# Kernel optimization log

Hardware: AMD Instinct MI355X
Metric: run time of the kernel (lower is better)

The kernel has to match this reference:

```python
import jax, jax.numpy as jnp
import numpy as np

NUM_HEADS = 32
HEAD_DIM = 128
HIDDEN = NUM_HEADS * HEAD_DIM  # 4096
PAGE_SIZE = 16
NUM_PHYS_PAGES = 512
CACHE_POS = 4096
BATCH = 32
SEQ = 1


def setup_inputs() -> dict:
    key = jax.random.key(0)
    ks = jax.random.split(key, 6)
    scale = 0.02
    x = jax.random.normal(ks[0], (BATCH, SEQ, HIDDEN), dtype=jnp.float32)
    w_qkv = jax.random.normal(ks[1], (HIDDEN, 3 * HIDDEN), dtype=jnp.float32) * scale
    b_qkv = jnp.zeros((3 * HIDDEN,), dtype=jnp.float32)
    w_proj = jax.random.normal(ks[2], (HIDDEN, HIDDEN), dtype=jnp.float32) * scale
    b_proj = jnp.zeros((HIDDEN,), dtype=jnp.float32)
    k_pages = jax.random.normal(ks[3], (NUM_PHYS_PAGES, PAGE_SIZE, NUM_HEADS, HEAD_DIM), dtype=jnp.float32)
    v_pages = jax.random.normal(ks[4], (NUM_PHYS_PAGES, PAGE_SIZE, NUM_HEADS, HEAD_DIM), dtype=jnp.float32)
    # logical page -> physical page mapping (page table for one request)
    page_table = jax.random.randint(ks[5], (CACHE_POS // PAGE_SIZE,), 0, NUM_PHYS_PAGES, dtype=jnp.int64)
    return {
        "x": x, "w_qkv": w_qkv, "b_qkv": b_qkv, "w_proj": w_proj, "b_proj": b_proj,
        "k_pages": k_pages, "v_pages": v_pages, "page_table": page_table,
        "cache_pos": CACHE_POS,
    }


def reference(x, w_qkv, b_qkv, w_proj, b_proj, k_pages, v_pages, page_table, cache_pos):
    B, S, H = x.shape
    # fused QKV projection
    qkv = x @ w_qkv + b_qkv                      # [B,S,3H]
    q, k, v = jnp.split(qkv, 3, axis=-1)
    q = q.reshape(B, S, NUM_HEADS, HEAD_DIM).transpose(0, 2, 1, 3)  # [B,Hh,S,D]
    k = k.reshape(B, S, NUM_HEADS, HEAD_DIM).transpose(0, 2, 1, 3)
    v = v.reshape(B, S, NUM_HEADS, HEAD_DIM).transpose(0, 2, 1, 3)

    # Paged KV-cache gather: position -> (physical page, local offset)
    pos = jnp.arange(cache_pos)                  # cache_pos is a static Python int
    phys = page_table[pos // PAGE_SIZE]          # [T]
    off = pos % PAGE_SIZE                        # [T]
    cached_k = k_pages[phys, off]                # [T, Hh, D]
    cached_v = v_pages[phys, off]                # [T, Hh, D]
    # [1,Hh,T,D], shared across batch (as in the torch expand)
    cached_k = jnp.transpose(cached_k, (1, 0, 2))[None]
    cached_v = jnp.transpose(cached_v, (1, 0, 2))[None]
    cached_k = jnp.broadcast_to(cached_k, (B,) + cached_k.shape[1:])
    cached_v = jnp.broadcast_to(cached_v, (B,) + cached_v.shape[1:])

    k_full = jnp.concatenate([cached_k, k], axis=2)  # [B,Hh,T+S,D]
    v_full = jnp.concatenate([cached_v, v], axis=2)

    scores = jnp.einsum('bhsd,bhtd->bhst', q, k_full) / (HEAD_DIM ** 0.5)
    attn = jax.nn.softmax(scores, axis=-1)
    out = jnp.einsum('bhst,bhtd->bhsd', attn, v_full)  # [B,Hh,S,D]
    out = out.transpose(0, 2, 1, 3).reshape(B, S, H)
    return out @ w_proj + b_proj
```

## Files before the change

### kernel.cpp

```cpp
#include <hip/hip_runtime.h>

typedef __attribute__((ext_vector_type(4))) float f32x4;
typedef __attribute__((ext_vector_type(8))) short short8;
typedef unsigned short u16;
typedef unsigned int u32;

#define HEADS 32
#define D 128
#define TCACHE 4096
#define HID 4096
#define QKVN 12288
#define TSPLIT 16
#define KPS (TCACHE / TSPLIT)
#define QKV_KSPLIT 4
#define PROJ_KSPLIT 8
#define SCALE 0.08838834764831845f
#define ARENA_W 10880

static __device__ __forceinline__ float bf2f(u16 u) {
  u32 v = ((u32)u) << 16;
  return __builtin_bit_cast(float, v);
}
static __device__ __forceinline__ u16 f2bf(float f) {
  u32 u = __builtin_bit_cast(u32, f);
  u += 0x7FFFu + ((u >> 16) & 1u);
  return (u16)(u >> 16);
}

template <bool BF>
static __device__ __forceinline__ short8 load8(const void* p, long idx) {
  if constexpr (BF) {
    return *(const short8*)((const u16*)p + idx);
  } else {
    const float* f = (const float*)p + idx;
    f32x4 a = *(const f32x4*)f;
    f32x4 b = *(const f32x4*)(f + 4);
    short8 r;
    r[0] = (short)f2bf(a[0]); r[1] = (short)f2bf(a[1]);
    r[2] = (short)f2bf(a[2]); r[3] = (short)f2bf(a[3]);
    r[4] = (short)f2bf(b[0]); r[5] = (short)f2bf(b[1]);
    r[6] = (short)f2bf(b[2]); r[7] = (short)f2bf(b[3]);
    return r;
  }
}
template <bool BF>
static __device__ __forceinline__ short ld1(const void* p, long idx) {
  if constexpr (BF) return (short)((const u16*)p)[idx];
  else return (short)f2bf(((const float*)p)[idx]);
}

__global__ void prep(const u32* __restrict__ x, const u32* __restrict__ raw,
                     int* __restrict__ flag, int* __restrict__ ptn) {
  if (blockIdx.x == 0) {
    __shared__ int cnt;
    if (threadIdx.x == 0) cnt = 0;
    __syncthreads();
    u32 v = x[threadIdx.x * 256];
    u32 e = (v >> 7) & 0xFF;
    if (e >= 110 && e <= 140) atomicAdd(&cnt, 1);
    __syncthreads();
    if (threadIdx.x == 0) *flag = (cnt >= 192) ? 1 : 0;
  } else {
    __shared__ int is64;
    if (threadIdx.x == 0) is64 = 1;
    __syncthreads();
    if (threadIdx.x < 128) {
      u32 odd = raw[2 * threadIdx.x + 1];
      if (odd != 0) atomicAnd(&is64, 0);
    }
    __syncthreads();
    if (is64) ptn[threadIdx.x] = (int)raw[2 * threadIdx.x];
    else ptn[threadIdx.x] = (int)raw[threadIdx.x];
  }
}

template <bool ABF, bool BBF>
static __device__ __forceinline__ void gemm_body(const void* __restrict__ A,
                                                 const void* __restrict__ B,
                                                 float* __restrict__ C, int K, int N) {
  int wave = threadIdx.x >> 6, lane = threadIdx.x & 63;
  int l16 = lane & 15, lg = lane >> 4;
  int n0 = blockIdx.x * 64 + wave * 16;
  int kper = K / gridDim.y;
  int k0 = blockIdx.y * kper;
  f32x4 acc0 = {0.f, 0.f, 0.f, 0.f}, acc1 = {0.f, 0.f, 0.f, 0.f};
  long arow0 = (long)l16 * K, arow1 = (long)(l16 + 16) * K;
#pragma unroll 4
  for (int kk = k0; kk < k0 + kper; kk += 32) {
    long kbase = kk + lg * 8;
    short8 a0 = load8<ABF>(A, arow0 + kbase);
    short8 a1 = load8<ABF>(A, arow1 + kbase);
    short8 bfr;
#pragma unroll
    for (int i = 0; i < 8; i++) bfr[i] = ld1<BBF>(B, (kbase + i) * (long)N + n0 + l16);
    acc0 = __builtin_amdgcn_mfma_f32_16x16x32_bf16(a0, bfr, acc0, 0, 0, 0);
    acc1 = __builtin_amdgcn_mfma_f32_16x16x32_bf16(a1, bfr, acc1, 0, 0, 0);
  }
  float* Co = C + (long)blockIdx.y * 32 * N;
#pragma unroll
  for (int i = 0; i < 4; i++) {
    int b = lg * 4 + i;
    Co[(long)b * N + n0 + l16] = acc0[i];
    Co[(long)(b + 16) * N + n0 + l16] = acc1[i];
  }
}

#define GPITCH 36
static __device__ __forceinline__ void gemm32_body(const float* __restrict__ A,
                                                   const float* __restrict__ B,
                                                   float* __restrict__ C, int K, int N,
                                                   u16* __restrict__ BtL,
                                                   u16* __restrict__ AtL) {
  int t = threadIdx.x;
  int wave = t >> 6, lane = t & 63, l16 = lane & 15, lg = lane >> 4;
  int kper = K / gridDim.y;
  int k0 = blockIdx.y * kper;
  int steps = kper >> 5;
  long n0 = (long)blockIdx.x * 64;
  int bk = (t >> 4) * 2;
  int bc = (t & 15) * 4;
  int am = t >> 3;
  int ak = (t & 7) * 4;
  f32x4 acc0 = {0.f, 0.f, 0.f, 0.f}, acc1 = {0.f, 0.f, 0.f, 0.f};
  f32x4 rb0, rb1, ra;

  auto LOADG = [&](int kk) {
    const float* Bp = B + (long)(k0 + kk + bk) * N + n0 + bc;
    rb0 = *(const f32x4*)Bp;
    rb1 = *(const f32x4*)(Bp + N);
    ra = *(const f32x4*)(A + (long)am * K + k0 + kk + ak);
  };
  auto STORE = [&](int buf) {
    u16* Bt = BtL + buf * (64 * GPITCH);
#pragma unroll
    for (int c = 0; c < 4; c++) {
      u32 w = (u32)f2bf(rb0[c]) | ((u32)f2bf(rb1[c]) << 16);
      *(u32*)(Bt + (bc + c) * GPITCH + bk) = w;
    }
    u16* At = AtL + buf * (32 * GPITCH);
    u32 w0 = (u32)f2bf(ra[0]) | ((u32)f2bf(ra[1]) << 16);
    u32 w1 = (u32)f2bf(ra[2]) | ((u32)f2bf(ra[3]) << 16);
    *(u32*)(At + am * GPITCH + ak) = w0;
    *(u32*)(At + am * GPITCH + ak + 2) = w1;
  };

  LOADG(0);
  STORE(0);
  __syncthreads();
  for (int s = 0; s < steps; s++) {
    int cur = s & 1;
    bool more = (s + 1 < steps);
    if (more) LOADG((s + 1) * 32);
    union { short8 s8; u32 w[4]; } bf, af0, af1;
    {
      const u32* bp = (const u32*)(BtL + cur * (64 * GPITCH) + ((wave * 16 + l16) * GPITCH + lg * 8));
      bf.w[0] = bp[0]; bf.w[1] = bp[1]; bf.w[2] = bp[2]; bf.w[3] = bp[3];
      const u32* a0p = (const u32*)(AtL + cur * (32 * GPITCH) + (l16 * GPITCH + lg * 8));
      af0.w[0] = a0p[0]; af0.w[1] = a0p[1]; af0.w[2] = a0p[2]; af0.w[3] = a0p[3];
      const u32* a1p = (const u32*)(AtL + cur * (32 * GPITCH) + ((l16 + 16) * GPITCH + lg * 8));
      af1.w[0] = a1p[0]; af1.w[1] = a1p[1]; af1.w[2] = a1p[2]; af1.w[3] = a1p[3];
    }
    acc0 = __builtin_amdgcn_mfma_f32_16x16x32_bf16(af0.s8, bf.s8, acc0, 0, 0, 0);
    acc1 = __builtin_amdgcn_mfma_f32_16x16x32_bf16(af1.s8, bf.s8, acc1, 0, 0, 0);
    if (more) STORE(cur ^ 1);
    __syncthreads();
  }
  float* Co = C + (long)blockIdx.y * 32 * N;
  long cw = n0 + wave * 16 + l16;
#pragma unroll
  for (int i = 0; i < 4; i++) {
    int b = lg * 4 + i;
    Co[(long)b * N + cw] = acc0[i];
    Co[(long)(b + 16) * N + cw] = acc1[i];
  }
}

__global__ __launch_bounds__(256) void qkv_gemm(const void* A, const void* B, float* C,
                                                const int* flag) {
  __shared__ u16 BtL[2 * 64 * GPITCH];
  __shared__ u16 AtL[2 * 32 * GPITCH];
  if (*flag) gemm_body<true, true>(A, B, C, HID, QKVN);
  else gemm32_body((const float*)A, (const float*)B, C, HID, QKVN, BtL, AtL);
}
__global__ __launch_bounds__(256) void proj_gemm(const void* Abf, const void* Af32,
                                                 const void* B, float* C, const int* flag) {
  __shared__ u16 BtL[2 * 64 * GPITCH];
  __shared__ u16 AtL[2 * 32 * GPITCH];
  if (*flag) gemm_body<true, true>(Abf, B, C, HID, HID);
  else gemm32_body((const float*)Af32, (const float*)B, C, HID, HID, BtL, AtL);
}

__global__ void qkv_fin(const float* __restrict__ C, const void* __restrict__ bias,
                        u16* __restrict__ out, const int* __restrict__ flag) {
  int idx = blockIdx.x * 256 + threadIdx.x;
  if (idx >= 32 * QKVN) return;
  int n = idx % QKVN;
  float s = 0.f;
#pragma unroll
  for (int sp = 0; sp < QKV_KSPLIT; sp++) s += C[(long)sp * 32 * QKVN + idx];
  float bv;
  if (*flag) bv = bf2f(((const u16*)bias)[n]);
  else bv = ((const float*)bias)[n];
  out[idx] = f2bf(s + bv);
}

__global__ void proj_fin(const float* __restrict__ C, const void* __restrict__ bias,
                         void* __restrict__ out, const int* __restrict__ flag) {
  int idx = blockIdx.x * 256 + threadIdx.x;
  if (idx >= 32 * HID) return;
  int n = idx % HID;
  float s = 0.f;
#pragma unroll
  for (int sp = 0; sp < PROJ_KSPLIT; sp++) s += C[(long)sp * 32 * HID + idx];
  if (*flag) {
    s += bf2f(((const u16*)bias)[n]);
    ((u16*)out)[idx] = f2bf(s);
  } else {
    s += ((const float*)bias)[n];
    ((float*)out)[idx] = s;
  }
}

template <bool BF>
static __device__ __forceinline__ void attn_body(const u16* __restrict__ qkv,
                                                 const void* __restrict__ kp,
                                                 const void* __restrict__ vp,
                                                 const int* __restrict__ pt,
                                                 float* __restrict__ Op,
                                                 float* __restrict__ mp,
                                                 float* __restrict__ lp,
                                                 char* __restrict__ arena,
                                                 float (*mL)[32], float (*lL)[32]) {
  int split = blockIdx.x, h = blockIdx.y;
  int wave = threadIdx.x >> 6, lane = threadIdx.x & 63;
  int l16 = lane & 15, lg = lane >> 4;
  u16* VLw = (u16*)(arena + wave * ARENA_W);
  u16* pldsw = (u16*)(arena + wave * ARENA_W + 8320);

  short8 qf[2][4];
#pragma unroll
  for (int mt = 0; mt < 2; mt++)
#pragma unroll
    for (int ks = 0; ks < 4; ks++)
      qf[mt][ks] = *(const short8*)(qkv + (long)(l16 + 16 * mt) * QKVN + h * D + ks * 32 + lg * 8);

  f32x4 acc[2][8];
#pragma unroll
  for (int mt = 0; mt < 2; mt++)
#pragma unroll
    for (int nt = 0; nt < 8; nt++) acc[mt][nt] = f32x4{0.f, 0.f, 0.f, 0.f};
  float mrun[2][4], lrun[2][4];
#pragma unroll
  for (int mt = 0; mt < 2; mt++)
#pragma unroll
    for (int i = 0; i < 4; i++) { mrun[mt][i] = -INFINITY; lrun[mt][i] = 0.f; }

  for (int c = 0; c < 2; c++) {
    int tbase = split * KPS + c * 128 + wave * 32;
    int tb16 = tbase >> 4;
    int pg0 = pt[tb16], pg1 = pt[tb16 + 1];

#pragma unroll
    for (int p = 0; p < 2; p++) {
      int kc = (lane >> 2) + p * 16;
      int dq = (lane & 3) * 32;
      int pg = (kc & 16) ? pg1 : pg0;
      long vr = ((long)(pg * 16 + (kc & 15)) * HEADS + h) * D;
      u32 w[16];
      if constexpr (BF) {
        const u32* src = (const u32*)vp + ((vr + dq) >> 1);
#pragma unroll
        for (int j = 0; j < 16; j++) w[j] = src[j];
      } else {
        const float* src = (const float*)vp + vr + dq;
#pragma unroll
        for (int j = 0; j < 8; j++) {
          f32x4 tv = *(const f32x4*)(src + j * 4);
          w[2 * j] = (u32)f2bf(tv[0]) | ((u32)f2bf(tv[1]) << 16);
          w[2 * j + 1] = (u32)f2bf(tv[2]) | ((u32)f2bf(tv[3]) << 16);
        }
      }
      u32* dst = (u32*)(VLw + kc * 130 + dq);
#pragma unroll
      for (int j = 0; j < 16; j++) dst[j] = w[j];
    }

    f32x4 sacc[2][2];
#pragma unroll
    for (int kt = 0; kt < 2; kt++)
#pragma unroll
      for (int mt = 0; mt < 2; mt++) sacc[kt][mt] = f32x4{0.f, 0.f, 0.f, 0.f};
#pragma unroll
    for (int kt = 0; kt < 2; kt++) {
      long krow = ((long)((kt ? pg1 : pg0) * 16 + l16) * HEADS + h) * D;
#pragma unroll
      for (int ks = 0; ks < 4; ks++) {
        short8 kf = load8<BF>(kp, krow + ks * 32 + lg * 8);
        sacc[kt][0] = __builtin_amdgcn_mfma_f32_16x16x32_bf16(qf[0][ks], kf, sacc[kt][0], 0, 0, 0);
        sacc[kt][1] = __builtin_amdgcn_mfma_f32_16x16x32_bf16(qf[1][ks], kf, sacc[kt][1], 0, 0, 0);
      }
    }

    float p[2][2][4];
#pragma unroll
    for (int mt = 0; mt < 2; mt++) {
#pragma unroll
      for (int i = 0; i < 4; i++) {
        float s0 = sacc[0][mt][i] * SCALE, s1 = sacc[1][mt][i] * SCALE;
        float mx = fmaxf(s0, s1);
        mx = fmaxf(mx, __shfl_xor(mx, 1));
        mx = fmaxf(mx, __shfl_xor(mx, 2));
        mx = fmaxf(mx, __shfl_xor(mx, 4));
        mx = fmaxf(mx, __shfl_xor(mx, 8));
        float mnew = fmaxf(mrun[mt][i], mx);
        float resc = __expf(mrun[mt][i] - mnew);
        float p0 = __expf(s0 - mnew), p1 = __expf(s1 - mnew);
        float ps = p0 + p1;
        ps += __shfl_xor(ps, 1);
        ps += __shfl_xor(ps, 2);
        ps += __shfl_xor(ps, 4);
        ps += __shfl_xor(ps, 8);
        mrun[mt][i] = mnew;
        lrun[mt][i] = lrun[mt][i] * resc + ps;
#pragma unroll
        for (int nt = 0; nt < 8; nt++) acc[mt][nt][i] *= resc;
        p[0][mt][i] = p0;
        p[1][mt][i] = p1;
      }
    }

#pragma unroll
    for (int kt = 0; kt < 2; kt++)
#pragma unroll
      for (int mt = 0; mt < 2; mt++)
#pragma unroll
        for (int i = 0; i < 4; i++)
          pldsw[(lg * 4 + i + 16 * mt) * 40 + kt * 16 + l16] = f2bf(p[kt][mt][i]);

    __syncthreads();

    short8 pf0 = *(const short8*)&pldsw[l16 * 40 + lg * 8];
    short8 pf1 = *(const short8*)&pldsw[(l16 + 16) * 40 + lg * 8];

#pragma unroll
    for (int nt = 0; nt < 8; nt++) {
      short8 vf;
#pragma unroll
      for (int i = 0; i < 8; i++) vf[i] = (short)VLw[(lg * 8 + i) * 130 + nt * 16 + l16];
      acc[0][nt] = __builtin_amdgcn_mfma_f32_16x16x32_bf16(pf0, vf, acc[0][nt], 0, 0, 0);
      acc[1][nt] = __builtin_amdgcn_mfma_f32_16x16x32_bf16(pf1, vf, acc[1][nt], 0, 0, 0);
    }
  }

  __syncthreads();

  u16* accw = (u16*)(arena + wave * ARENA_W);
#pragma unroll
  for (int mt = 0; mt < 2; mt++)
#pragma unroll
    for (int i = 0; i < 4; i++) {
      int b = lg * 4 + i + 16 * mt;
#pragma unroll
      for (int nt = 0; nt < 8; nt++) accw[b * D + nt * 16 + l16] = f2bf(acc[mt][nt][i]);
      if (l16 == 0) {
        mL[wave][b] = mrun[mt][i];
        lL[wave][b] = lrun[mt][i];
      }
    }
  __syncthreads();

  long sb = ((long)h * TSPLIT + split) * 32;
  {
    int t = threadIdx.x;
    int b = t >> 3, sub = t & 7;
    float m0 = mL[0][b], m1 = mL[1][b], m2 = mL[2][b], m3 = mL[3][b];
    float ms = fmaxf(fmaxf(m0, m1), fmaxf(m2, m3));
    float w0 = __expf(m0 - ms), w1 = __expf(m1 - ms);
    float w2 = __expf(m2 - ms), w3 = __expf(m3 - ms);
    float ls = lL[0][b] * w0 + lL[1][b] * w1 + lL[2][b] * w2 + lL[3][b] * w3;
    const u16* a0 = (const u16*)(arena);
    const u16* a1 = (const u16*)(arena + ARENA_W);
    const u16* a2 = (const u16*)(arena + 2 * ARENA_W);
    const u16* a3 = (const u16*)(arena + 3 * ARENA_W);
    long ob = (sb + b) * (long)D;
#pragma unroll
    for (int j = 0; j < 16; j++) {
      int d = sub + 8 * j;
      int idx = b * D + d;
      float o = bf2f(a0[idx]) * w0 + bf2f(a1[idx]) * w1 + bf2f(a2[idx]) * w2 + bf2f(a3[idx]) * w3;
      Op[ob + d] = o;
    }
    if (sub == 0) {
      mp[sb + b] = ms;
      lp[sb + b] = ls;
    }
  }
}

__global__ __launch_bounds__(256) void attn_partial(const u16* qkv, const void* kp,
                                                    const void* vp, const int* pt,
                                                    const int* flag, float* Op, float* mp,
                                                    float* lp) {
  __shared__ __align__(16) char arena[4 * ARENA_W];
  __shared__ float mL[4][32], lL[4][32];
  if (*flag) attn_body<true>(qkv, kp, vp, pt, Op, mp, lp, arena, mL, lL);
  else attn_body<false>(qkv, kp, vp, pt, Op, mp, lp, arena, mL, lL);
}

__global__ __launch_bounds__(64) void attn_combine(const u16* __restrict__ qkv,
                                                   const float* __restrict__ Op,
                                                   const float* __restrict__ mp,
                                                   const float* __restrict__ lp,
                                                   u16* __restrict__ aout,
                                                   float* __restrict__ aoutf) {
  int bh = blockIdx.x;
  int b = bh >> 5, h = bh & 31;
  int lane = threadIdx.x;
  long qb = (long)b * QKVN + h * D + 2 * lane;
  float q0 = bf2f(qkv[qb]), q1 = bf2f(qkv[qb + 1]);
  float k0 = bf2f(qkv[qb + HID]), k1 = bf2f(qkv[qb + HID + 1]);
  float v0 = bf2f(qkv[qb + 2 * HID]), v1 = bf2f(qkv[qb + 2 * HID + 1]);
  float dot = q0 * k0 + q1 * k1;
#pragma unroll
  for (int m = 1; m < 64; m <<= 1) dot += __shfl_xor(dot, m);
  float scur = dot * SCALE;
  long base = (long)h * TSPLIT * 32 + b;
  float M = scur;
#pragma unroll
  for (int s = 0; s < TSPLIT; s++) M = fmaxf(M, mp[base + s * 32]);
  float w = __expf(scur - M), L = w, o0 = w * v0, o1 = w * v1;
#pragma unroll
  for (int s = 0; s < TSPLIT; s++) {
    float wsx = __expf(mp[base + s * 32] - M);
    L += lp[base + s * 32] * wsx;
    const float* o = Op + (base + s * 32) * D + 2 * lane;
    o0 += wsx * o[0];
    o1 += wsx * o[1];
  }
  float inv = 1.0f / L;
  o0 *= inv;
  o1 *= inv;
  long oi = (long)b * HID + h * D + 2 * lane;
  u32 pk = (u32)f2bf(o0) | ((u32)f2bf(o1) << 16);
  *(u32*)(aout + oi) = pk;
  aoutf[oi] = o0;
  aoutf[oi + 1] = o1;
}

extern "C" void kernel_launch(void* const* d_in, const int* in_sizes, int n_in, void* d_out,
                              int out_size, void* d_ws, size_t ws_size, hipStream_t stream) {
  const void* x = d_in[0];
  const void* wqkv = d_in[1];
  const void* bqkv = d_in[2];
  const void* wproj = d_in[3];
  const void* bproj = d_in[4];
  const void* kp = d_in[5];
  const void* vp = d_in[6];
  const u32* ptraw = (const u32*)d_in[7];

  char* wsb = (char*)d_ws;
  int* flag = (int*)(wsb + 0);
  int* ptn = (int*)(wsb + 16);
  float* qkv_part = (float*)(wsb + 2048);
  float* proj_part = qkv_part;
  float* attn_f32 = (float*)(wsb + 2048 + 4194304);
  u16* qkv_bf = (u16*)(wsb + 6293504);
  float* Opart = (float*)(wsb + 7079936);
  float* mpart = (float*)(wsb + 15468544);
  float* lpart = (float*)(wsb + 15534080);
  u16* attn_bf = (u16*)(wsb + 15599616);

  prep<<<2, 256, 0, stream>>>((const u32*)x, ptraw, flag, ptn);
  qkv_gemm<<<dim3(QKVN / 64, QKV_KSPLIT), 256, 0, stream>>>(x, wqkv, qkv_part, flag);
  qkv_fin<<<(32 * QKVN) / 256, 256, 0, stream>>>(qkv_part, bqkv, qkv_bf, flag);
  attn_partial<<<dim3(TSPLIT, HEADS), 256, 0, stream>>>(qkv_bf, kp, vp, ptn, flag, Opart,
                                                        mpart, lpart);
  attn_combine<<<32 * 32, 64, 0, stream>>>(qkv_bf, Opart, mpart, lpart, attn_bf, attn_f32);
  proj_gemm<<<dim3(HID / 64, PROJ_KSPLIT), 256, 0, stream>>>(attn_bf, attn_f32, wproj,
                                                             proj_part, flag);
  proj_fin<<<(32 * HID) / 256, 256, 0, stream>>>(proj_part, bproj, d_out, flag);
}
```

Before: 127.1 us.

## Double register prefetch in fp32 GEMM and raise projection K-split

The fp32 GEMM main loop now keeps two sets of global-load registers, so loads for step s+2 and s+3 are issued two steps ahead of the MFMA that consumes them. The goal is to hide more global-memory latency behind compute. The projection GEMM K-split goes from 8 to 16 to launch more blocks. Workspace offsets are moved so the larger projection partial buffer no longer overlaps other buffers. The changes cost more registers, and the larger K-split adds partial-sum traffic in proj_fin.

```diff
diff --git a/kernel.cpp b/kernel.cpp
--- a/kernel.cpp
+++ b/kernel.cpp
@@ -13,7 +13,7 @@
 #define TSPLIT 16
 #define KPS (TCACHE / TSPLIT)
 #define QKV_KSPLIT 4
-#define PROJ_KSPLIT 8
+#define PROJ_KSPLIT 16
 #define SCALE 0.08838834764831845f
 #define ARENA_W 10880
 
@@ -122,47 +122,66 @@
   int am = t >> 3;
   int ak = (t & 7) * 4;
   f32x4 acc0 = {0.f, 0.f, 0.f, 0.f}, acc1 = {0.f, 0.f, 0.f, 0.f};
-  f32x4 rb0, rb1, ra;
-
-  auto LOADG = [&](int kk) {
+  f32x4 rb0A, rb1A, raA, rb0B, rb1B, raB;
+
+  auto LOADGA = [&](int kk) {
     const float* Bp = B + (long)(k0 + kk + bk) * N + n0 + bc;
-    rb0 = *(const f32x4*)Bp;
-    rb1 = *(const f32x4*)(Bp + N);
-    ra = *(const f32x4*)(A + (long)am * K + k0 + kk + ak);
+    rb0A = *(const f32x4*)Bp;
+    rb1A = *(const f32x4*)(Bp + N);
+    raA = *(const f32x4*)(A + (long)am * K + k0 + kk + ak);
   };
-  auto STORE = [&](int buf) {
+  auto LOADGB = [&](int kk) {
+    const float* Bp = B + (long)(k0 + kk + bk) * N + n0 + bc;
+    rb0B = *(const f32x4*)Bp;
+    rb1B = *(const f32x4*)(Bp + N);
+    raB = *(const f32x4*)(A + (long)am * K + k0 + kk + ak);
+  };
+  auto STOREA = [&](int buf) {
     u16* Bt = BtL + buf * (64 * GPITCH);
 #pragma unroll
     for (int c = 0; c < 4; c++) {
-      u32 w = (u32)f2bf(rb0[c]) | ((u32)f2bf(rb1[c]) << 16);
+      u32 w = (u32)f2bf(rb0A[c]) | ((u32)f2bf(rb1A[c]) << 16);
       *(u32*)(Bt + (bc + c) * GPITCH + bk) = w;
     }
     u16* At = AtL + buf * (32 * GPITCH);
-    u32 w0 = (u32)f2bf(ra[0]) | ((u32)f2bf(ra[1]) << 16);
-    u32 w1 = (u32)f2bf(ra[2]) | ((u32)f2bf(ra[3]) << 16);
-    *(u32*)(At + am * GPITCH + ak) = w0;
-    *(u32*)(At + am * GPITCH + ak + 2) = w1;
+    *(u32*)(At + am * GPITCH + ak) = (u32)f2bf(raA[0]) | ((u32)f2bf(raA[1]) << 16);
+    *(u32*)(At + am * GPITCH + ak + 2) = (u32)f2bf(raA[2]) | ((u32)f2bf(raA[3]) << 16);
   };
-
-  LOADG(0);
-  STORE(0);
-  __syncthreads();
-  for (int s = 0; s < steps; s++) {
-    int cur = s & 1;
-    bool more = (s + 1 < steps);
-    if (more) LOADG((s + 1) * 32);
+  auto STOREB = [&](int buf) {
+    u16* Bt = BtL + buf * (64 * GPITCH);
+#pragma unroll
+    for (int c = 0; c < 4; c++) {
+      u32 w = (u32)f2bf(rb0B[c]) | ((u32)f2bf(rb1B[c]) << 16);
+      *(u32*)(Bt + (bc + c) * GPITCH + bk) = w;
+    }
+    u16* At = AtL + buf * (32 * GPITCH);
+    *(u32*)(At + am * GPITCH + ak) = (u32)f2bf(raB[0]) | ((u32)f2bf(raB[1]) << 16);
+    *(u32*)(At + am * GPITCH + ak + 2) = (u32)f2bf(raB[2]) | ((u32)f2bf(raB[3]) << 16);
+  };
+  auto FRAGMFMA = [&](int buf) {
     union { short8 s8; u32 w[4]; } bf, af0, af1;
-    {
-      const u32* bp = (const u32*)(BtL + cur * (64 * GPITCH) + ((wave * 16 + l16) * GPITCH + lg * 8));
-      bf.w[0] = bp[0]; bf.w[1] = bp[1]; bf.w[2] = bp[2]; bf.w[3] = bp[3];
-      const u32* a0p = (const u32*)(AtL + cur * (32 * GPITCH) + (l16 * GPITCH + lg * 8));
-      af0.w[0] = a0p[0]; af0.w[1] = a0p[1]; af0.w[2] = a0p[2]; af0.w[3] = a0p[3];
-      const u32* a1p = (const u32*)(AtL + cur * (32 * GPITCH) + ((l16 + 16) * GPITCH + lg * 8));
-      af1.w[0] = a1p[0]; af1.w[1] = a1p[1]; af1.w[2] = a1p[2]; af1.w[3] = a1p[3];
-    }
+    const u32* bp = (const u32*)(BtL + buf * (64 * GPITCH) + ((wave * 16 + l16) * GPITCH + lg * 8));
+    bf.w[0] = bp[0]; bf.w[1] = bp[1]; bf.w[2] = bp[2]; bf.w[3] = bp[3];
+    const u32* a0p = (const u32*)(AtL + buf * (32 * GPITCH) + (l16 * GPITCH + lg * 8));
+    af0.w[0] = a0p[0]; af0.w[1] = a0p[1]; af0.w[2] = a0p[2]; af0.w[3] = a0p[3];
+    const u32* a1p = (const u32*)(AtL + buf * (32 * GPITCH) + ((l16 + 16) * GPITCH + lg * 8));
+    af1.w[0] = a1p[0]; af1.w[1] = a1p[1]; af1.w[2] = a1p[2]; af1.w[3] = a1p[3];
     acc0 = __builtin_amdgcn_mfma_f32_16x16x32_bf16(af0.s8, bf.s8, acc0, 0, 0, 0);
     acc1 = __builtin_amdgcn_mfma_f32_16x16x32_bf16(af1.s8, bf.s8, acc1, 0, 0, 0);
-    if (more) STORE(cur ^ 1);
+  };
+
+  LOADGA(0);
+  LOADGB(32);
+  STOREA(0);
+  __syncthreads();
+  for (int s = 0; s < steps; s += 2) {
+    if (s + 2 < steps) LOADGA((s + 2) * 32);
+    FRAGMFMA(0);
+    STOREB(1);
+    __syncthreads();
+    if (s + 3 < steps) LOADGB((s + 3) * 32);
+    FRAGMFMA(1);
+    if (s + 2 < steps) STOREA(0);
     __syncthreads();
   }
   float* Co = C + (long)blockIdx.y * 32 * N;
@@ -462,13 +481,13 @@
   int* flag = (int*)(wsb + 0);
   int* ptn = (int*)(wsb + 16);
   float* qkv_part = (float*)(wsb + 2048);
-  float* proj_part = qkv_part;
-  float* attn_f32 = (float*)(wsb + 2048 + 4194304);
   u16* qkv_bf = (u16*)(wsb + 6293504);
   float* Opart = (float*)(wsb + 7079936);
   float* mpart = (float*)(wsb + 15468544);
   float* lpart = (float*)(wsb + 15534080);
   u16* attn_bf = (u16*)(wsb + 15599616);
+  float* attn_f32 = (float*)(wsb + 15861760);
+  float* proj_part = (float*)(wsb + 16777216);
 
   prep<<<2, 256, 0, stream>>>((const u32*)x, ptraw, flag, ptn);
   qkv_gemm<<<dim3(QKVN / 64, QKV_KSPLIT), 256, 0, stream>>>(x, wqkv, qkv_part, flag);
```

Result: no change. 128.7 us (+1.3%).

## Double K-step per iteration and raise split-K for QKV and projection GEMMs

Applied to the files above, without the earlier changes.

The fp32 GEMM path now stages 64 K-elements per iteration as two 32-wide LDS sub-tiles, issuing twice as many loads in flight and halving the barrier count per K. Split-K factors are doubled for both GEMMs to put more blocks on the device, with launch bounds requesting 4 blocks per SM. The workspace is re-laid out so the larger partial buffers no longer overlap. The cost is more partial-sum traffic in the finalize kernels, plus more registers and LDS per block.

```diff
diff --git a/kernel.cpp b/kernel.cpp
--- a/kernel.cpp
+++ b/kernel.cpp
@@ -12,10 +12,12 @@
 #define QKVN 12288
 #define TSPLIT 16
 #define KPS (TCACHE / TSPLIT)
-#define QKV_KSPLIT 4
-#define PROJ_KSPLIT 8
+#define QKV_KSPLIT 8
+#define PROJ_KSPLIT 16
 #define SCALE 0.08838834764831845f
 #define ARENA_W 10880
+#define GP 36
+#define BK 64
 
 static __device__ __forceinline__ float bf2f(u16 u) {
   u32 v = ((u32)u) << 16;
@@ -105,7 +107,6 @@
   }
 }
 
-#define GPITCH 36
 static __device__ __forceinline__ void gemm32_body(const float* __restrict__ A,
                                                    const float* __restrict__ B,
                                                    float* __restrict__ C, int K, int N,
@@ -115,33 +116,50 @@
   int wave = t >> 6, lane = t & 63, l16 = lane & 15, lg = lane >> 4;
   int kper = K / gridDim.y;
   int k0 = blockIdx.y * kper;
-  int steps = kper >> 5;
+  int steps = kper / BK;
   long n0 = (long)blockIdx.x * 64;
   int bk = (t >> 4) * 2;
   int bc = (t & 15) * 4;
   int am = t >> 3;
   int ak = (t & 7) * 4;
   f32x4 acc0 = {0.f, 0.f, 0.f, 0.f}, acc1 = {0.f, 0.f, 0.f, 0.f};
-  f32x4 rb0, rb1, ra;
+  f32x4 rb0[2], rb1[2], ra[2];
 
   auto LOADG = [&](int kk) {
-    const float* Bp = B + (long)(k0 + kk + bk) * N + n0 + bc;
-    rb0 = *(const f32x4*)Bp;
-    rb1 = *(const f32x4*)(Bp + N);
-    ra = *(const f32x4*)(A + (long)am * K + k0 + kk + ak);
+#pragma unroll
+    for (int sub = 0; sub < 2; sub++) {
+      const float* Bp = B + (long)(k0 + kk + sub * 32 + bk) * N + n0 + bc;
+      rb0[sub] = *(const f32x4*)Bp;
+      rb1[sub] = *(const f32x4*)(Bp + N);
+      ra[sub] = *(const f32x4*)(A + (long)am * K + k0 + kk + sub * 32 + ak);
+    }
   };
   auto STORE = [&](int buf) {
-    u16* Bt = BtL + buf * (64 * GPITCH);
-#pragma unroll
-    for (int c = 0; c < 4; c++) {
-      u32 w = (u32)f2bf(rb0[c]) | ((u32)f2bf(rb1[c]) << 16);
-      *(u32*)(Bt + (bc + c) * GPITCH + bk) = w;
-    }
-    u16* At = AtL + buf * (32 * GPITCH);
-    u32 w0 = (u32)f2bf(ra[0]) | ((u32)f2bf(ra[1]) << 16);
-    u32 w1 = (u32)f2bf(ra[2]) | ((u32)f2bf(ra[3]) << 16);
-    *(u32*)(At + am * GPITCH + ak) = w0;
-    *(u32*)(At + am * GPITCH + ak + 2) = w1;
+#pragma unroll
+    for (int sub = 0; sub < 2; sub++) {
+      u16* Bt = BtL + (buf * 2 + sub) * (64 * GP);
+#pragma unroll
+      for (int c = 0; c < 4; c++) {
+        u32 w = (u32)f2bf(rb0[sub][c]) | ((u32)f2bf(rb1[sub][c]) << 16);
+        *(u32*)(Bt + (bc + c) * GP + bk) = w;
+      }
+      u16* At = AtL + (buf * 2 + sub) * (32 * GP);
+      *(u32*)(At + am * GP + ak) = (u32)f2bf(ra[sub][0]) | ((u32)f2bf(ra[sub][1]) << 16);
+      *(u32*)(At + am * GP + ak + 2) = (u32)f2bf(ra[sub][2]) | ((u32)f2bf(ra[sub][3]) << 16);
+    }
+  };
+  auto FRAGMFMA = [&](int buf, int sub) {
+    union { short8 s8; u32 w[4]; } bf, af0, af1;
+    const u32* bp = (const u32*)(BtL + (buf * 2 + sub) * (64 * GP) +
+                                 ((wave * 16 + l16) * GP + lg * 8));
+    bf.w[0] = bp[0]; bf.w[1] = bp[1]; bf.w[2] = bp[2]; bf.w[3] = bp[3];
+    const u32* a0p = (const u32*)(AtL + (buf * 2 + sub) * (32 * GP) + (l16 * GP + lg * 8));
+    af0.w[0] = a0p[0]; af0.w[1] = a0p[1]; af0.w[2] = a0p[2]; af0.w[3] = a0p[3];
+    const u32* a1p = (const u32*)(AtL + (buf * 2 + sub) * (32 * GP) +
+                                  ((l16 + 16) * GP + lg * 8));
+    af1.w[0] = a1p[0]; af1.w[1] = a1p[1]; af1.w[2] = a1p[2]; af1.w[3] = a1p[3];
+    acc0 = __builtin_amdgcn_mfma_f32_16x16x32_bf16(af0.s8, bf.s8, acc0, 0, 0, 0);
+    acc1 = __builtin_amdgcn_mfma_f32_16x16x32_bf16(af1.s8, bf.s8, acc1, 0, 0, 0);
   };
 
   LOADG(0);
@@ -150,18 +168,9 @@
   for (int s = 0; s < steps; s++) {
     int cur = s & 1;
     bool more = (s + 1 < steps);
-    if (more) LOADG((s + 1) * 32);
-    union { short8 s8; u32 w[4]; } bf, af0, af1;
-    {
-      const u32* bp = (const u32*)(BtL + cur * (64 * GPITCH) + ((wave * 16 + l16) * GPITCH + lg * 8));
-      bf.w[0] = bp[0]; bf.w[1] = bp[1]; bf.w[2] = bp[2]; bf.w[3] = bp[3];
-      const u32* a0p = (const u32*)(AtL + cur * (32 * GPITCH) + (l16 * GPITCH + lg * 8));
-      af0.w[0] = a0p[0]; af0.w[1] = a0p[1]; af0.w[2] = a0p[2]; af0.w[3] = a0p[3];
-      const u32* a1p = (const u32*)(AtL + cur * (32 * GPITCH) + ((l16 + 16) * GPITCH + lg * 8));
-      af1.w[0] = a1p[0]; af1.w[1] = a1p[1]; af1.w[2] = a1p[2]; af1.w[3] = a1p[3];
-    }
-    acc0 = __builtin_amdgcn_mfma_f32_16x16x32_bf16(af0.s8, bf.s8, acc0, 0, 0, 0);
-    acc1 = __builtin_amdgcn_mfma_f32_16x16x32_bf16(af1.s8, bf.s8, acc1, 0, 0, 0);
+    if (more) LOADG((s + 1) * BK);
+    FRAGMFMA(cur, 0);
+    FRAGMFMA(cur, 1);
     if (more) STORE(cur ^ 1);
     __syncthreads();
   }
@@ -175,17 +184,17 @@
   }
 }
 
-__global__ __launch_bounds__(256) void qkv_gemm(const void* A, const void* B, float* C,
-                                                const int* flag) {
-  __shared__ u16 BtL[2 * 64 * GPITCH];
-  __shared__ u16 AtL[2 * 32 * GPITCH];
+__global__ __launch_bounds__(256, 4) void qkv_gemm(const void* A, const void* B, float* C,
+                                                   const int* flag) {
+  __shared__ u16 BtL[2 * 2 * 64 * GP];
+  __shared__ u16 AtL[2 * 2 * 32 * GP];
   if (*flag) gemm_body<true, true>(A, B, C, HID, QKVN);
   else gemm32_body((const float*)A, (const float*)B, C, HID, QKVN, BtL, AtL);
 }
-__global__ __launch_bounds__(256) void proj_gemm(const void* Abf, const void* Af32,
-                                                 const void* B, float* C, const int* flag) {
-  __shared__ u16 BtL[2 * 64 * GPITCH];
-  __shared__ u16 AtL[2 * 32 * GPITCH];
+__global__ __launch_bounds__(256, 4) void proj_gemm(const void* Abf, const void* Af32,
+                                                    const void* B, float* C, const int* flag) {
+  __shared__ u16 BtL[2 * 2 * 64 * GP];
+  __shared__ u16 AtL[2 * 2 * 32 * GP];
   if (*flag) gemm_body<true, true>(Abf, B, C, HID, HID);
   else gemm32_body((const float*)Af32, (const float*)B, C, HID, HID, BtL, AtL);
 }
@@ -462,13 +471,13 @@
   int* flag = (int*)(wsb + 0);
   int* ptn = (int*)(wsb + 16);
   float* qkv_part = (float*)(wsb + 2048);
-  float* proj_part = qkv_part;
-  float* attn_f32 = (float*)(wsb + 2048 + 4194304);
-  u16* qkv_bf = (u16*)(wsb + 6293504);
-  float* Opart = (float*)(wsb + 7079936);
-  float* mpart = (float*)(wsb + 15468544);
-  float* lpart = (float*)(wsb + 15534080);
-  u16* attn_bf = (u16*)(wsb + 15599616);
+  u16* qkv_bf = (u16*)(wsb + 12584960);
+  float* Opart = (float*)(wsb + 13371392);
+  float* mpart = (float*)(wsb + 21760000);
+  float* lpart = (float*)(wsb + 21825536);
+  u16* attn_bf = (u16*)(wsb + 21891072);
+  float* attn_f32 = (float*)(wsb + 22153216);
+  float* proj_part = (float*)(wsb + 22677504);
 
   prep<<<2, 256, 0, stream>>>((const u32*)x, ptraw, flag, ptn);
   qkv_gemm<<<dim3(QKVN / 64, QKV_KSPLIT), 256, 0, stream>>>(x, wqkv, qkv_part, flag);
```

Result: slower. 135.3 us (+6.4%).
